# Optimization experiments

Measured on AMD Instinct MI355X. Metric: run time of the kernel, lower is better.

Reference implementation:

```python
import jax, jax.numpy as jnp
import numpy as np
import math

EMBED_DIM = 128
NUM_HEADS = 8
TANH_CLIP = 10.0
L, N, S, E = 1, 1024, 2000, 128


def setup_inputs() -> dict:
    key = jax.random.key(0)
    ks = jax.random.split(key, 7)
    query = jax.random.normal(ks[0], (L, N, E), dtype=jnp.float32)
    glimpse_K = jax.random.normal(ks[1], (S, N, E), dtype=jnp.float32)
    glimpse_V = jax.random.normal(ks[2], (S, N, E), dtype=jnp.float32)
    logit_K = jax.random.normal(ks[3], (N, S, E), dtype=jnp.float32)
    attn_mask = jax.random.randint(ks[4], (N, L, S), 0, 2).astype(jnp.bool_)
    # glimpse_proj params (nn.Linear: y = x @ W.T + b)
    lim = 1.0 / math.sqrt(E)
    W = jax.random.uniform(ks[5], (E, E), dtype=jnp.float32, minval=-lim, maxval=lim)
    b = jax.random.uniform(ks[6], (E,), dtype=jnp.float32, minval=-lim, maxval=lim)
    return {"query": query, "glimpse_K": glimpse_K, "glimpse_V": glimpse_V,
            "logit_K": logit_K, "attn_mask": attn_mask, "W": W, "b": b}


def reference(query, glimpse_K, glimpse_V, logit_K, attn_mask, W, b):
    H = NUM_HEADS
    tgt_len, bsz, embed_dim = query.shape
    src_len = glimpse_K.shape[0]
    head_dim = embed_dim // H
    neg_min = jnp.finfo(query.dtype).min

    # (L,N,E) -> (H,N,L,hd)
    gQ = query.reshape(tgt_len, bsz, H, head_dim).transpose(2, 1, 0, 3)
    gK = glimpse_K.reshape(src_len, bsz, H, head_dim).transpose(2, 1, 0, 3)
    gV = glimpse_V.reshape(src_len, bsz, H, head_dim).transpose(2, 1, 0, 3)

    # compatibility: (H,N,L,S)
    comp = jnp.einsum('hnld,hnsd->hnls', gQ, gK) / math.sqrt(head_dim)
    comp = jnp.where(attn_mask[None], neg_min, comp)  # broadcast mask over heads

    heads = jnp.einsum('hnls,hnsd->hnld', jax.nn.softmax(comp, axis=-1), gV)
    # (H,N,L,hd) -> (N,L,E)
    glimpse = heads.transpose(1, 2, 0, 3).reshape(bsz, tgt_len, embed_dim)
    final_Q = glimpse @ W.T + b

    logits = jnp.einsum('nle,nse->nls', final_Q, logit_K) / math.sqrt(embed_dim)
    logits = jnp.tanh(logits) * TANH_CLIP
    logits = jnp.where(attn_mask, neg_min, logits)
    log_prob = jax.nn.log_softmax(logits, axis=-1)  # (N,L,S)
    return log_prob.squeeze(1)
```

## Files before the change

kernel.cpp:

```cpp
#include <hip/hip_runtime.h>
#include <cfloat>
#include <math.h>

#define NB      1024
#define SLEN    2000
#define EDIM    128
#define NWAVES  4
#define NSTREAM (NWAVES * 2)
#define SENT    (-1e30f)
#define MASKED_OUT (-3.3895313892515355e38f)

__global__ __launch_bounds__(256, 4)
void attn_decoder_kernel(const float* __restrict__ query,
                         const float* __restrict__ gK,
                         const float* __restrict__ gV,
                         const float* __restrict__ lK,
                         const unsigned char* __restrict__ mask,
                         const float* __restrict__ W,
                         const float* __restrict__ bias,
                         float* __restrict__ out)
{
    const int n    = blockIdx.x;
    const int tid  = threadIdx.x;
    const int wave = tid >> 6;
    const int lane = tid & 63;
    const int half = lane >> 5;
    const int l5   = lane & 31;

    __shared__ float sm[NSTREAM][8];
    __shared__ float sl[NSTREAM][8];
    __shared__ float sacc[NSTREAM][EDIM];
    __shared__ float glimpse[EDIM];
    __shared__ float finalQ[EDIM];
    __shared__ float logits_sh[SLEN];
    __shared__ unsigned char mask_sh[SLEN];
    __shared__ float smB[NSTREAM], slB[NSTREAM];

    for (int i = tid; i < SLEN; i += 256)
        mask_sh[i] = mask[(size_t)n * SLEN + i];

    const float4 q4 = ((const float4*)(query + (size_t)n * EDIM))[l5];

    __syncthreads();

    float  mh = SENT, lh = 0.f;
    float4 acc = make_float4(0.f, 0.f, 0.f, 0.f);

    #pragma unroll 1
    for (int it = 0; it < SLEN / 16; ++it) {
        const int r0 = it * 16 + wave * 4;
        const int sA = r0 + half;
        const int sB = r0 + 2 + half;
        const size_t offA = ((size_t)sA * NB + n) * EDIM + l5 * 4;
        const size_t offB = ((size_t)sB * NB + n) * EDIM + l5 * 4;
        const float4 kA = *(const float4*)(gK + offA);
        const float4 vA = *(const float4*)(gV + offA);
        const float4 kB = *(const float4*)(gK + offB);
        const float4 vB = *(const float4*)(gV + offB);

        {
            float d = fmaf(q4.x, kA.x, fmaf(q4.y, kA.y, fmaf(q4.z, kA.z, q4.w * kA.w)));
            d += __shfl_xor(d, 1);
            d += __shfl_xor(d, 2);
            const float comp = mask_sh[sA] ? SENT : d * 0.25f;
            const float mn = fmaxf(mh, comp);
            const float scale = __expf(mh - mn);
            const float p     = __expf(comp - mn);
            lh = fmaf(lh, scale, p);
            acc.x = fmaf(acc.x, scale, p * vA.x);
            acc.y = fmaf(acc.y, scale, p * vA.y);
            acc.z = fmaf(acc.z, scale, p * vA.z);
            acc.w = fmaf(acc.w, scale, p * vA.w);
            mh = mn;
        }
        {
            float d = fmaf(q4.x, kB.x, fmaf(q4.y, kB.y, fmaf(q4.z, kB.z, q4.w * kB.w)));
            d += __shfl_xor(d, 1);
            d += __shfl_xor(d, 2);
            const float comp = mask_sh[sB] ? SENT : d * 0.25f;
            const float mn = fmaxf(mh, comp);
            const float scale = __expf(mh - mn);
            const float p     = __expf(comp - mn);
            lh = fmaf(lh, scale, p);
            acc.x = fmaf(acc.x, scale, p * vB.x);
            acc.y = fmaf(acc.y, scale, p * vB.y);
            acc.z = fmaf(acc.z, scale, p * vB.z);
            acc.w = fmaf(acc.w, scale, p * vB.w);
            mh = mn;
        }
    }

    {
        const int st = wave * 2 + half;
        if ((l5 & 3) == 0) { sm[st][l5 >> 2] = mh; sl[st][l5 >> 2] = lh; }
        ((float4*)sacc[st])[l5] = acc;
    }
    __syncthreads();

    if (tid < EDIM) {
        const int hh = tid >> 4;
        float M = sm[0][hh];
        #pragma unroll
        for (int st = 1; st < NSTREAM; ++st) M = fmaxf(M, sm[st][hh]);
        float L = 0.f, a = 0.f;
        #pragma unroll
        for (int st = 0; st < NSTREAM; ++st) {
            const float f = __expf(sm[st][hh] - M);
            L = fmaf(sl[st][hh], f, L);
            a = fmaf(sacc[st][tid], f, a);
        }
        glimpse[tid] = a / fmaxf(L, 1e-30f);
    }
    __syncthreads();

    {
        const int e  = tid & 127;
        const int k0 = (tid >> 7) * 64;
        const float* Wrow = W + (size_t)e * EDIM + k0;
        const float* g = glimpse + k0;
        float sum = 0.f;
        #pragma unroll 16
        for (int k = 0; k < 64; ++k) sum = fmaf(g[k], Wrow[k], sum);
        ((float*)sacc)[tid] = sum;
    }
    __syncthreads();
    if (tid < EDIM)
        finalQ[tid] = ((float*)sacc)[tid] + ((float*)sacc)[tid + 128] + bias[tid];
    __syncthreads();

    const float4 fq4 = ((const float4*)finalQ)[l5];
    float mB = SENT, lB = 0.f;
    const float* lbase = lK + (size_t)n * SLEN * EDIM;

    #pragma unroll 1
    for (int it = 0; it < SLEN / 16; ++it) {
        const int r0 = it * 16 + wave * 4;
        const float4 tA = *(const float4*)(lbase + (size_t)r0 * EDIM + lane * 4);
        const float4 tB = *(const float4*)(lbase + (size_t)(r0 + 2) * EDIM + lane * 4);

        {
            float d = fmaf(fq4.x, tA.x, fmaf(fq4.y, tA.y, fmaf(fq4.z, tA.z, fq4.w * tA.w)));
            d += __shfl_xor(d, 1);
            d += __shfl_xor(d, 2);
            d += __shfl_xor(d, 4);
            d += __shfl_xor(d, 8);
            d += __shfl_xor(d, 16);
            const int s = r0 + half;
            if (!mask_sh[s]) {
                const float x = d * 0.08838834764831845f;
                const float e = __expf(-2.f * fabsf(x));
                const float logit = copysignf(10.f * (1.f - e) / (1.f + e), x);
                if (l5 == 0) logits_sh[s] = logit;
                const float mn = fmaxf(mB, logit);
                lB = fmaf(lB, __expf(mB - mn), __expf(logit - mn));
                mB = mn;
            }
        }
        {
            float d = fmaf(fq4.x, tB.x, fmaf(fq4.y, tB.y, fmaf(fq4.z, tB.z, fq4.w * tB.w)));
            d += __shfl_xor(d, 1);
            d += __shfl_xor(d, 2);
            d += __shfl_xor(d, 4);
            d += __shfl_xor(d, 8);
            d += __shfl_xor(d, 16);
            const int s = r0 + 2 + half;
            if (!mask_sh[s]) {
                const float x = d * 0.08838834764831845f;
                const float e = __expf(-2.f * fabsf(x));
                const float logit = copysignf(10.f * (1.f - e) / (1.f + e), x);
                if (l5 == 0) logits_sh[s] = logit;
                const float mn = fmaxf(mB, logit);
                lB = fmaf(lB, __expf(mB - mn), __expf(logit - mn));
                mB = mn;
            }
        }
    }

    {
        const int st = wave * 2 + half;
        if (l5 == 0) { smB[st] = mB; slB[st] = lB; }
    }
    __syncthreads();

    float M = smB[0];
    #pragma unroll
    for (int st = 1; st < NSTREAM; ++st) M = fmaxf(M, smB[st]);
    float L = 0.f;
    #pragma unroll
    for (int st = 0; st < NSTREAM; ++st) L = fmaf(slB[st], __expf(smB[st] - M), L);
    const float lse = (L > 0.f) ? (M + logf(L)) : 0.f;

    float* orow = out + (size_t)n * SLEN;
    for (int i = tid; i < SLEN; i += 256)
        orow[i] = mask_sh[i] ? MASKED_OUT : (logits_sh[i] - lse);
}

extern "C" void kernel_launch(void* const* d_in, const int* in_sizes, int n_in,
                              void* d_out, int out_size, void* d_ws, size_t ws_size,
                              hipStream_t stream) {
    const float*         query = (const float*)d_in[0];
    const float*         gK    = (const float*)d_in[1];
    const float*         gV    = (const float*)d_in[2];
    const float*         lK    = (const float*)d_in[3];
    const unsigned char* mask  = (const unsigned char*)d_in[4];
    const float*         W     = (const float*)d_in[5];
    const float*         bias  = (const float*)d_in[6];
    float*               out   = (float*)d_out;

    attn_decoder_kernel<<<dim3(NB), dim3(256), 0, stream>>>(
        query, gK, gV, lK, mask, W, bias, out);
}
```

Before: 552.4 us.

## Compact unmasked source indices and skip loading masked K/V/logit rows

```diff
diff --git a/kernel.cpp b/kernel.cpp
--- a/kernel.cpp
+++ b/kernel.cpp
@@ -34,7 +34,9 @@
     __shared__ float finalQ[EDIM];
     __shared__ float logits_sh[SLEN];
     __shared__ unsigned char mask_sh[SLEN];
+    __shared__ unsigned short idx_sh[SLEN];
     __shared__ float smB[NSTREAM], slB[NSTREAM];
+    __shared__ int wave_tot[NWAVES];
 
     for (int i = tid; i < SLEN; i += 256)
         mask_sh[i] = mask[(size_t)n * SLEN + i];
@@ -43,14 +45,47 @@
 
     __syncthreads();
 
+    int mycnt = 0;
+    const int s0c = tid * 8;
+    #pragma unroll
+    for (int k = 0; k < 8; ++k) {
+        const int s = s0c + k;
+        if (s < SLEN && !mask_sh[s]) mycnt++;
+    }
+    int inc = mycnt;
+    #pragma unroll
+    for (int off = 1; off < 64; off <<= 1) {
+        const int v = __shfl_up(inc, off);
+        if (lane >= off) inc += v;
+    }
+    if (lane == 63) wave_tot[wave] = inc;
+    __syncthreads();
+    int wbase = 0;
+    #pragma unroll
+    for (int w = 0; w < NWAVES; ++w) if (w < wave) wbase += wave_tot[w];
+    const int C = wave_tot[0] + wave_tot[1] + wave_tot[2] + wave_tot[3];
+    int pos = wbase + inc - mycnt;
+    #pragma unroll
+    for (int k = 0; k < 8; ++k) {
+        const int s = s0c + k;
+        if (s < SLEN && !mask_sh[s]) idx_sh[pos++] = (unsigned short)s;
+    }
+    __syncthreads();
+
+    const int nIt = (C + 15) >> 4;
+
     float  mh = SENT, lh = 0.f;
     float4 acc = make_float4(0.f, 0.f, 0.f, 0.f);
 
     #pragma unroll 1
-    for (int it = 0; it < SLEN / 16; ++it) {
-        const int r0 = it * 16 + wave * 4;
-        const int sA = r0 + half;
-        const int sB = r0 + 2 + half;
+    for (int it = 0; it < nIt; ++it) {
+        const int j0 = it * 16 + wave * 4;
+        const int jA = j0 + half;
+        const int jB = j0 + 2 + half;
+        const bool pA = jA < C;
+        const bool pB = jB < C;
+        const int sA = idx_sh[pA ? jA : 0];
+        const int sB = idx_sh[pB ? jB : 0];
         const size_t offA = ((size_t)sA * NB + n) * EDIM + l5 * 4;
         const size_t offB = ((size_t)sB * NB + n) * EDIM + l5 * 4;
         const float4 kA = *(const float4*)(gK + offA);
@@ -62,7 +97,7 @@
             float d = fmaf(q4.x, kA.x, fmaf(q4.y, kA.y, fmaf(q4.z, kA.z, q4.w * kA.w)));
             d += __shfl_xor(d, 1);
             d += __shfl_xor(d, 2);
-            const float comp = mask_sh[sA] ? SENT : d * 0.25f;
+            const float comp = pA ? d * 0.25f : SENT;
             const float mn = fmaxf(mh, comp);
             const float scale = __expf(mh - mn);
             const float p     = __expf(comp - mn);
@@ -77,7 +112,7 @@
             float d = fmaf(q4.x, kB.x, fmaf(q4.y, kB.y, fmaf(q4.z, kB.z, q4.w * kB.w)));
             d += __shfl_xor(d, 1);
             d += __shfl_xor(d, 2);
-            const float comp = mask_sh[sB] ? SENT : d * 0.25f;
+            const float comp = pB ? d * 0.25f : SENT;
             const float mn = fmaxf(mh, comp);
             const float scale = __expf(mh - mn);
             const float p     = __expf(comp - mn);
@@ -133,10 +168,16 @@
     const float* lbase = lK + (size_t)n * SLEN * EDIM;
 
     #pragma unroll 1
-    for (int it = 0; it < SLEN / 16; ++it) {
-        const int r0 = it * 16 + wave * 4;
-        const float4 tA = *(const float4*)(lbase + (size_t)r0 * EDIM + lane * 4);
-        const float4 tB = *(const float4*)(lbase + (size_t)(r0 + 2) * EDIM + lane * 4);
+    for (int it = 0; it < nIt; ++it) {
+        const int j0 = it * 16 + wave * 4;
+        const int jA = j0 + half;
+        const int jB = j0 + 2 + half;
+        const bool pA = jA < C;
+        const bool pB = jB < C;
+        const int sA = idx_sh[pA ? jA : 0];
+        const int sB = idx_sh[pB ? jB : 0];
+        const float4 tA = *(const float4*)(lbase + (size_t)sA * EDIM + l5 * 4);
+        const float4 tB = *(const float4*)(lbase + (size_t)sB * EDIM + l5 * 4);
 
         {
             float d = fmaf(fq4.x, tA.x, fmaf(fq4.y, tA.y, fmaf(fq4.z, tA.z, fq4.w * tA.w)));
@@ -145,12 +186,11 @@
             d += __shfl_xor(d, 4);
             d += __shfl_xor(d, 8);
             d += __shfl_xor(d, 16);
-            const int s = r0 + half;
-            if (!mask_sh[s]) {
+            if (pA) {
                 const float x = d * 0.08838834764831845f;
                 const float e = __expf(-2.f * fabsf(x));
                 const float logit = copysignf(10.f * (1.f - e) / (1.f + e), x);
-                if (l5 == 0) logits_sh[s] = logit;
+                if (l5 == 0) logits_sh[sA] = logit;
                 const float mn = fmaxf(mB, logit);
                 lB = fmaf(lB, __expf(mB - mn), __expf(logit - mn));
                 mB = mn;
@@ -163,12 +203,11 @@
             d += __shfl_xor(d, 4);
             d += __shfl_xor(d, 8);
             d += __shfl_xor(d, 16);
-            const int s = r0 + 2 + half;
-            if (!mask_sh[s]) {
+            if (pB) {
                 const float x = d * 0.08838834764831845f;
                 const float e = __expf(-2.f * fabsf(x));
                 const float logit = copysignf(10.f * (1.f - e) / (1.f + e), x);
-                if (l5 == 0) logits_sh[s] = logit;
+                if (l5 == 0) logits_sh[sB] = logit;
                 const float mn = fmaxf(mB, logit);
                 lB = fmaf(lB, __expf(mB - mn), __expf(logit - mn));
                 mB = mn;
```

Result: faster. 485.5 us (-12.1%).
